# Kernel tuning notes

Hardware: AMD Instinct MI355X
Metric: run time of the kernel (lower is better)

Reference implementation:

```python
import jax, jax.numpy as jnp
import numpy as np

# Model dims
B, N, D_MODEL, N_HEADS = 8, 4096, 512, 8
EXPAND = 2
D1 = (EXPAND * D_MODEL) // N_HEADS * N_HEADS      # 1024
HEAD_DIM = D1 // N_HEADS                          # 128
RANK, NK = 32, 16
GAMMA = 0.999


def setup_inputs() -> dict:
    key = jax.random.key(0)
    ks = jax.random.split(key, 24)

    def p(i, shape, std=0.02):
        return std * jax.random.normal(ks[i], shape, dtype=jnp.float32)

    def toep_params(i0):
        # SKI low-rank Toeplitz operator params: kernel values at NK inducing
        # lag positions, factorized as (h, nk, r) @ (h, r, d), plus lag-0 term.
        return (p(i0, (N_HEADS, 1, HEAD_DIM), 1.0),        # zero lag
                p(i0 + 1, (N_HEADS, NK, RANK), 0.1),       # pos lags A
                p(i0 + 2, (N_HEADS, RANK, HEAD_DIM), 0.1), # pos lags B
                p(i0 + 3, (N_HEADS, NK, RANK), 0.1),       # neg lags A
                p(i0 + 4, (N_HEADS, RANK, HEAD_DIM), 0.1)) # neg lags B

    t1 = toep_params(7)
    t2 = toep_params(12)
    return {
        'x': jax.random.normal(ks[0], (B, N, D_MODEL), dtype=jnp.float32),
        'u_w': p(1, (D1, D_MODEL)), 'u_b': p(2, (D1,)),
        'v_w': p(3, (D1, D_MODEL)), 'v_b': p(4, (D1,)),
        'o_w': p(5, (D_MODEL, D1)), 'o_b': p(6, (D_MODEL,)),
        't1_zero': t1[0], 't1_pa': t1[1], 't1_pb': t1[2], 't1_na': t1[3], 't1_nb': t1[4],
        't2_zero': t2[0], 't2_pa': t2[1], 't2_pb': t2[2], 't2_na': t2[3], 't2_nb': t2[4],
    }


def _build_kernel(zero, pos_a, pos_b, neg_a, neg_b, n):
    """Build circular-conv kernel a of shape (h, 2n, d): a[k]=t(k), a[2n-k]=t(-k)."""
    h, nk, _ = pos_a.shape
    d = pos_b.shape[-1]
    tm_pos = jnp.einsum('hkr,hrd->hkd', pos_a, pos_b)   # kernel at inducing lags
    tm_neg = jnp.einsum('hkr,hrd->hkd', neg_a, neg_b)
    lags = jnp.arange(1, n, dtype=jnp.float32)          # lags 1..n-1
    # linear interpolation from NK inducing points to n-1 lags
    pos_f = (lags - 1.0) / max(n - 2, 1) * (nk - 1)
    lo = jnp.floor(pos_f).astype(jnp.int32)
    hi = jnp.minimum(lo + 1, nk - 1)
    w = (pos_f - lo)[None, :, None]
    decay = (GAMMA ** lags)[None, :, None]              # exponential decay bias
    t_pos = ((1.0 - w) * tm_pos[:, lo] + w * tm_pos[:, hi]) * decay
    t_neg = ((1.0 - w) * tm_neg[:, lo] + w * tm_neg[:, hi]) * decay
    return jnp.concatenate(
        [zero, t_pos, jnp.zeros((h, 1, d), t_pos.dtype), jnp.flip(t_neg, axis=1)],
        axis=1)


def _toep_apply(x, zero, pos_a, pos_b, neg_a, neg_b):
    # x: (b, n, g) with g = h*d; multi-head Toeplitz mixing along axis 1 via FFT.
    b, n, g = x.shape
    h = zero.shape[0]
    d = g // h
    xh = x.reshape(b, n, h, d).transpose(0, 2, 1, 3)    # (b, h, n, d)
    a = _build_kernel(zero, pos_a, pos_b, neg_a, neg_b, n)  # (h, 2n, d)
    y = jnp.fft.irfft(
        jnp.fft.rfft(xh, 2 * n, axis=2) * jnp.fft.rfft(a, axis=1)[None],
        2 * n, axis=2)[:, :, :n]
    return y.transpose(0, 2, 1, 3).reshape(b, n, g)


def reference(x, u_w, u_b, v_w, v_b, o_w, o_b,
              t1_zero, t1_pa, t1_pb, t1_na, t1_nb,
              t2_zero, t2_pa, t2_pb, t2_na, t2_nb):
    b, n, _ = x.shape
    H = int(np.sqrt(n))
    W = n // H
    u = jax.nn.silu(x @ u_w.T + u_b)
    v = jax.nn.silu(x @ v_w.T + v_b)
    g = v.shape[-1]
    t1 = (t1_zero, t1_pa, t1_pb, t1_na, t1_nb)
    t2 = (t2_zero, t2_pa, t2_pb, t2_na, t2_nb)
    # path 1: mix along W (rows) with toep1, then along H (cols) with toep2
    o1 = _toep_apply(v.reshape(b * H, W, g), *t1)
    o1 = o1.reshape(b, H, W, g).transpose(0, 2, 1, 3).reshape(b * W, H, g)
    o1 = _toep_apply(o1, *t2)
    o1 = o1.reshape(b, W, H, g).transpose(0, 2, 1, 3).reshape(b, H * W, g)
    # path 2: mix along H with toep2, then along W with toep1
    v2 = v.reshape(b, H, W, g).transpose(0, 2, 1, 3).reshape(b * W, H, g)
    o2 = _toep_apply(v2, *t2)
    o2 = o2.reshape(b, W, H, g).transpose(0, 2, 1, 3).reshape(b * H, W, g)
    o2 = _toep_apply(o2, *t1)
    o2 = o2.reshape(b, H * W, g)
    # SiLU gate + output projection
    return (u * (o1 + o2)) @ o_w.T + o_b
```

## Files before the change

### kernel.cpp

```cpp
#include <hip/hip_runtime.h>
#include <hip/hip_bf16.h>
#include <hip/hip_fp16.h>

typedef __bf16 bf16;
typedef bf16 bf16x2 __attribute__((ext_vector_type(2)));
typedef bf16 bf16x4 __attribute__((ext_vector_type(4)));
typedef bf16 bf16x8 __attribute__((ext_vector_type(8)));
typedef float f32x2 __attribute__((ext_vector_type(2)));
typedef float f32x4 __attribute__((ext_vector_type(4)));

__device__ __forceinline__ void gload_lds16(const void* g, void* l) {
  __builtin_amdgcn_global_load_lds((__attribute__((address_space(1))) void*)g,
                                   (__attribute__((address_space(3))) void*)l,
                                   16, 0, 0);
}

__device__ __forceinline__ f32x2 fma2(f32x2 a, f32x2 b, f32x2 c) {
  return __builtin_elementwise_fma(a, b, c);
}

__device__ __forceinline__ f32x2 cvt2(unsigned int u) {
  __half2 h = *(__half2*)&u;
  float2 f = __half22float2(h);
  f32x2 r = {f.x, f.y};
  return r;
}


__global__ void cast_f32_to_bf16(const float* __restrict__ in, bf16* __restrict__ out, int n4) {
  int i = blockIdx.x * blockDim.x + threadIdx.x;
  if (i >= n4) return;
  float4 v = ((const float4*)in)[i];
  bf16x4 o = {(bf16)v.x, (bf16)v.y, (bf16)v.z, (bf16)v.w};
  ((bf16x4*)out)[i] = o;
}

__global__ void cast_w3(const float* __restrict__ uw, const float* __restrict__ vw,
                        const float* __restrict__ ow,
                        bf16* __restrict__ wuv, bf16* __restrict__ owb) {
  int t = blockIdx.x * 256 + threadIdx.x;
  int r = t >> 17;
  int i = t & 131071;
  const float* src = (r == 0) ? uw : (r == 1) ? vw : ow;
  bf16* dst = (r == 2) ? owb : (wuv + (r == 1) * 524288);
  float4 v = ((const float4*)src)[i];
  bf16x4 o = {(bf16)v.x, (bf16)v.y, (bf16)v.z, (bf16)v.w};
  ((bf16x4*)dst)[i] = o;
}

__global__ void concat_bias(const float* __restrict__ ub, const float* __restrict__ vb,
                            float* __restrict__ buv) {
  int i = blockIdx.x * blockDim.x + threadIdx.x;
  if (i < 1024) { buv[i] = ub[i]; buv[1024 + i] = vb[i]; }
}

__global__ void build_tkp(const float* __restrict__ zero, const float* __restrict__ pa,
                          const float* __restrict__ pb, const float* __restrict__ na,
                          const float* __restrict__ nb, unsigned int* __restrict__ Tkp,
                          float scale) {
  int idx = blockIdx.x * blockDim.x + threadIdx.x;
  if (idx >= 8 * 127 * 64) return;
  int cp = idx & 63;
  int lagIdx = (idx >> 6) % 127;
  int h = idx / (64 * 127);
  int lag = lagIdx - 63;
  float t0, t1;
  if (lag == 0) {
    t0 = zero[h * 128 + 2 * cp];
    t1 = zero[h * 128 + 2 * cp + 1];
  } else {
    int k = lag > 0 ? lag : -lag;
    const float* A  = lag > 0 ? pa : na;
    const float* Bm = lag > 0 ? pb : nb;
    float pos_f = (float)(k - 1) * (15.0f / 62.0f);
    int lo = (int)floorf(pos_f);
    int hi = min(lo + 1, 15);
    float w = pos_f - (float)lo;
    float s0 = 0.f, s1 = 0.f;
    for (int r = 0; r < 32; ++r) {
      float c = (1.f - w) * A[(h * 16 + lo) * 32 + r] + w * A[(h * 16 + hi) * 32 + r];
      s0 += c * Bm[(h * 32 + r) * 128 + 2 * cp];
      s1 += c * Bm[(h * 32 + r) * 128 + 2 * cp + 1];
    }
    float dec = powf(0.999f, (float)k);
    t0 = s0 * dec;
    t1 = s1 * dec;
  }
  __half2 hv = __floats2half2_rn(t0 * scale, t1 * scale);
  Tkp[idx] = *(unsigned int*)&hv;
}


template<int MODE>
__global__ __launch_bounds__(256)
void gemm_bt(const bf16* __restrict__ A, const bf16* __restrict__ B,
             const float* __restrict__ bias,
             bf16* __restrict__ out_u, bf16* __restrict__ out_v,
             float* __restrict__ out_f,
             int M, int N, int K) {
  __shared__ bf16 As[128 * 32];
  __shared__ bf16 Bs[128 * 32];
  const int tid  = threadIdx.x;
  const int lane = tid & 63;
  const int nbn  = N >> 7;
  const int cpx  = gridDim.x >> 3;
  const int swz  = (blockIdx.x & 7) * cpx + (blockIdx.x >> 3);
  const int br   = (swz / nbn) << 7;
  const int bc   = (swz % nbn) << 7;
  const int wub  = __builtin_amdgcn_readfirstlane(tid & 192);

  f32x4 acc[4][4] = {};

  auto stage = [&](int k0) {
#pragma unroll
    for (int r = 0; r < 2; ++r) {
      const int flat = r * 256 + tid;
      const int row  = flat >> 2;
      const int kc   = (flat & 3) << 3;
      gload_lds16(A + ((size_t)(br + row) * K + k0 + kc),
                  (char*)As + (size_t)(r * 256 + wub) * 16);
      gload_lds16(B + ((size_t)(bc + row) * K + k0 + kc),
                  (char*)Bs + (size_t)(r * 256 + wub) * 16);
    }
  };

  const int l15 = lane & 15;
  const int lk  = (lane >> 4) << 3;
  const int wr  = ((tid >> 7) & 1) << 6;
  const int wc  = ((tid >> 6) & 1) << 6;

  auto compute = [&]() {
    bf16x8 af[4], bfr[4];
#pragma unroll
    for (int m = 0; m < 4; ++m)
      af[m] = *(const bf16x8*)&As[(wr + m * 16 + l15) * 32 + lk];
#pragma unroll
    for (int n = 0; n < 4; ++n)
      bfr[n] = *(const bf16x8*)&Bs[(wc + n * 16 + l15) * 32 + lk];
#pragma unroll
    for (int m = 0; m < 4; ++m)
#pragma unroll
      for (int n = 0; n < 4; ++n)
        acc[m][n] = __builtin_amdgcn_mfma_f32_16x16x32_bf16(af[m], bfr[n], acc[m][n], 0, 0, 0);
  };

  stage(0);
  __syncthreads();
  for (int k0 = 32; k0 < K; k0 += 32) {
    compute();
    __syncthreads();
    stage(k0);
    __syncthreads();
  }
  compute();

  const int lr4 = (lane >> 4) << 2;
  if (MODE == 0) {
    const bool isU = (bc < 1024);
    bf16* outp = isU ? out_u : out_v;
#pragma unroll
    for (int m = 0; m < 4; ++m) {
#pragma unroll
      for (int n = 0; n < 4; ++n) {
        const int col  = bc + wc + n * 16 + l15;
        const int ocol = (bc & 1023) + wc + n * 16 + l15;
        const float bv = bias[col];
#pragma unroll
        for (int r = 0; r < 4; ++r) {
          const int row = br + wr + m * 16 + lr4 + r;
          float xv = acc[m][n][r] + bv;
          float s  = xv / (1.f + __expf(-xv));
          outp[(size_t)row * 1024 + ocol] = (bf16)s;
        }
      }
    }
  } else {
#pragma unroll
    for (int m = 0; m < 4; ++m) {
#pragma unroll
      for (int n = 0; n < 4; ++n) {
        const int col  = bc + wc + n * 16 + l15;
        const float bv = bias[col];
#pragma unroll
        for (int r = 0; r < 4; ++r) {
          const int row = br + wr + m * 16 + lr4 + r;
          out_f[(size_t)row * N + col] = acc[m][n][r] + bv;
        }
      }
    }
  }
}


template<int FUSE>
__global__ __launch_bounds__(256)
void toep_pass(const bf16* __restrict__ in, const unsigned int* __restrict__ Tkp,
               const bf16* __restrict__ ufuse, bf16* __restrict__ out,
               int stride_j, int stride_row) {
  __shared__ unsigned int tkl[8192];
  __shared__ bf16 vbuf[64 * 132];
  const int tid    = threadIdx.x;
  const int rowIdx = blockIdx.x >> 3;
  const int head   = blockIdx.x & 7;
  const size_t base = (size_t)(rowIdx >> 6) * 4194304
                    + (size_t)(rowIdx & 63) * stride_row + head * 128;

  {
    const unsigned int* tg = Tkp + head * 8128;
    const int wub = __builtin_amdgcn_readfirstlane(tid & 192);
#pragma unroll
    for (int it = 0; it < 8; ++it) {
      const int flat = it * 256 + tid;
      gload_lds16(tg + flat * 4, (char*)tkl + (size_t)(it * 256 + wub) * 16);
    }
  }
#pragma unroll
  for (int it = 0; it < 2; ++it) {
    int c  = it * 256 + tid;
    int j  = c >> 3;
    int cg = c & 7;
    const bf16* p = in + base + (size_t)j * stride_j + cg * 16;
    bf16x8 a0 = *(const bf16x8*)p;
    bf16x8 a1 = *(const bf16x8*)(p + 8);
    *(bf16x8*)&vbuf[j * 132 + cg * 16]     = a0;
    *(bf16x8*)&vbuf[j * 132 + cg * 16 + 8] = a1;
  }
  __syncthreads();

  const int lane = tid & 63;
  const int i0   = (tid >> 6) << 4;
  f32x2 acc[16] = {};

  for (int jb = 0; jb < 4; ++jb) {
    f32x2 t[31];
    const int tbase = (i0 - 16 * jb + 48) * 64 + lane;
#pragma unroll
    for (int s = 0; s < 31; ++s) t[s] = cvt2(tkl[tbase + s * 64]);
#pragma unroll
    for (int jj = 0; jj < 16; ++jj) {
      unsigned int vu = *(const unsigned int*)&vbuf[(jb * 16 + jj) * 132 + (lane << 1)];
      f32x2 v2;
      v2.x = __uint_as_float(vu << 16);
      v2.y = __uint_as_float(vu & 0xFFFF0000u);
#pragma unroll
      for (int ii = 0; ii < 16; ++ii)
        acc[ii] = fma2(t[ii - jj + 15], v2, acc[ii]);
    }
  }

  const int d0 = lane << 1;
#pragma unroll
  for (int ii = 0; ii < 16; ++ii) {
    const size_t oidx = base + (size_t)(i0 + ii) * stride_j + d0;
    float a0 = acc[ii].x, a1 = acc[ii].y;
    if (FUSE) {
      bf16x2 uu = *(const bf16x2*)(ufuse + oidx);
      a0 *= (float)uu[0];
      a1 *= (float)uu[1];
    }
    bf16x2 o2 = {(bf16)a0, (bf16)a1};
    *(bf16x2*)(out + oidx) = o2;
  }
}


extern "C" void kernel_launch(void* const* d_in, const int* in_sizes, int n_in,
                              void* d_out, int out_size, void* d_ws, size_t ws_size,
                              hipStream_t stream) {
  const float* x    = (const float*)d_in[0];
  const float* u_w  = (const float*)d_in[1];
  const float* u_b  = (const float*)d_in[2];
  const float* v_w  = (const float*)d_in[3];
  const float* v_b  = (const float*)d_in[4];
  const float* o_w  = (const float*)d_in[5];
  const float* o_b  = (const float*)d_in[6];
  const float* t1z  = (const float*)d_in[7];
  const float* t1pa = (const float*)d_in[8];
  const float* t1pb = (const float*)d_in[9];
  const float* t1na = (const float*)d_in[10];
  const float* t1nb = (const float*)d_in[11];
  const float* t2z  = (const float*)d_in[12];
  const float* t2pa = (const float*)d_in[13];
  const float* t2pb = (const float*)d_in[14];
  const float* t2na = (const float*)d_in[15];
  const float* t2nb = (const float*)d_in[16];

  char* ws = (char*)d_ws;
  size_t off = 0;
  auto alloc = [&](size_t bytes) {
    char* p = ws + off;
    off += (bytes + 255) & ~(size_t)255;
    return p;
  };
  bf16*  xb   = (bf16*)alloc(32768ull * 512 * 2);
  bf16*  wuv  = (bf16*)alloc(2048ull * 512 * 2);
  bf16*  owb  = (bf16*)alloc(512ull * 1024 * 2);
  float* buv  = (float*)alloc(2048ull * 4);
  unsigned int* Tkp1 = (unsigned int*)alloc(8ull * 127 * 64 * 4 + 256);
  unsigned int* Tkp2 = (unsigned int*)alloc(8ull * 127 * 64 * 4 + 256);
  bf16*  u    = (bf16*)alloc(32768ull * 1024 * 2);
  bf16*  v    = (bf16*)alloc(32768ull * 1024 * 2);
  bf16*  tmid = (bf16*)alloc(32768ull * 1024 * 2);
  bf16*  g    = v;

  cast_f32_to_bf16<<<16384, 256, 0, stream>>>(x, xb, 16777216 / 4);
  cast_w3<<<1536, 256, 0, stream>>>(u_w, v_w, o_w, wuv, owb);
  concat_bias<<<4, 256, 0, stream>>>(u_b, v_b, buv);
  build_tkp<<<254, 256, 0, stream>>>(t1z, t1pa, t1pb, t1na, t1nb, Tkp1, 1.0f);
  build_tkp<<<254, 256, 0, stream>>>(t2z, t2pa, t2pb, t2na, t2nb, Tkp2, 2.0f);

  gemm_bt<0><<<4096, 256, 0, stream>>>(xb, wuv, buv, u, v, nullptr, 32768, 2048, 512);
  toep_pass<0><<<4096, 256, 0, stream>>>(v, Tkp1, nullptr, tmid, 1024, 65536);
  toep_pass<1><<<4096, 256, 0, stream>>>(tmid, Tkp2, u, g, 65536, 1024);
  gemm_bt<1><<<1024, 256, 0, stream>>>(g, owb, o_b, nullptr, nullptr, (float*)d_out,
                                       32768, 512, 1024);
}
```

Baseline: 309.0 us.

## Fuse first Toeplitz pass into the U/V projection GEMM epilogue

The V half of the input projection GEMM now keeps the SiLU-activated 128x128 tile in LDS and applies the first Toeplitz mixing pass directly, writing tmid instead of a full v buffer. This removes one kernel launch and a full write and read of the 32768x1024 v tensor. Each block's 128 rows hold two 64-row image rows, so the row-wise Toeplitz mixing can run within a single tile. The change also adds launch_bounds occupancy hints to both kernels, at the cost of a heavier GEMM epilogue with high register pressure and tail work only in the V blocks.

```diff
diff --git a/kernel.cpp b/kernel.cpp
--- a/kernel.cpp
+++ b/kernel.cpp
@@ -91,13 +91,143 @@
 }
 
 
-template<int MODE>
+#define VP 132
+
+__global__ __launch_bounds__(256, 3)
+void gemm_uvt(const bf16* __restrict__ A, const bf16* __restrict__ B,
+              const float* __restrict__ bias, const unsigned int* __restrict__ Tkp1,
+              bf16* __restrict__ out_u, bf16* __restrict__ tmid) {
+  __shared__ __align__(16) char smem[2 * 64 * VP * 2];
+  bf16* As = (bf16*)smem;
+  bf16* Bs = (bf16*)(smem + 8192);
+  bf16* vls = (bf16*)smem;
+  const int K = 512;
+  const int tid  = threadIdx.x;
+  const int lane = tid & 63;
+  const int cpx  = gridDim.x >> 3;
+  const int swz  = (blockIdx.x & 7) * cpx + (blockIdx.x >> 3);
+  const int br   = (swz >> 4) << 7;
+  const int bc   = (swz & 15) << 7;
+  const int wub  = __builtin_amdgcn_readfirstlane(tid & 192);
+
+  f32x4 acc[4][4] = {};
+
+  auto stage = [&](int k0) {
+#pragma unroll
+    for (int r = 0; r < 2; ++r) {
+      const int flat = r * 256 + tid;
+      const int row  = flat >> 2;
+      const int kc   = (flat & 3) << 3;
+      gload_lds16(A + ((size_t)(br + row) * K + k0 + kc),
+                  (char*)As + (size_t)(r * 256 + wub) * 16);
+      gload_lds16(B + ((size_t)(bc + row) * K + k0 + kc),
+                  (char*)Bs + (size_t)(r * 256 + wub) * 16);
+    }
+  };
+
+  const int l15 = lane & 15;
+  const int lk  = (lane >> 4) << 3;
+  const int wr  = ((tid >> 7) & 1) << 6;
+  const int wc  = ((tid >> 6) & 1) << 6;
+
+  auto compute = [&]() {
+    bf16x8 af[4], bfr[4];
+#pragma unroll
+    for (int m = 0; m < 4; ++m)
+      af[m] = *(const bf16x8*)&As[(wr + m * 16 + l15) * 32 + lk];
+#pragma unroll
+    for (int n = 0; n < 4; ++n)
+      bfr[n] = *(const bf16x8*)&Bs[(wc + n * 16 + l15) * 32 + lk];
+#pragma unroll
+    for (int m = 0; m < 4; ++m)
+#pragma unroll
+      for (int n = 0; n < 4; ++n)
+        acc[m][n] = __builtin_amdgcn_mfma_f32_16x16x32_bf16(af[m], bfr[n], acc[m][n], 0, 0, 0);
+  };
+
+  stage(0);
+  __syncthreads();
+  for (int k0 = 32; k0 < K; k0 += 32) {
+    compute();
+    __syncthreads();
+    stage(k0);
+    __syncthreads();
+  }
+  compute();
+  __syncthreads();
+
+  const int lr4 = (lane >> 4) << 2;
+  if (bc < 1024) {
+#pragma unroll
+    for (int m = 0; m < 4; ++m) {
+#pragma unroll
+      for (int n = 0; n < 4; ++n) {
+        const int col = bc + wc + n * 16 + l15;
+        const float bv = bias[col];
+#pragma unroll
+        for (int r = 0; r < 4; ++r) {
+          const int row = br + wr + m * 16 + lr4 + r;
+          float xv = acc[m][n][r] + bv;
+          float s  = xv / (1.f + __expf(-xv));
+          out_u[(size_t)row * 1024 + col] = (bf16)s;
+        }
+      }
+    }
+  } else {
+    const int head = (bc - 1024) >> 7;
+#pragma unroll
+    for (int m = 0; m < 4; ++m) {
+#pragma unroll
+      for (int n = 0; n < 4; ++n) {
+        const int col = wc + n * 16 + l15;
+        const float bv = bias[bc + col];
+#pragma unroll
+        for (int r = 0; r < 4; ++r) {
+          const int rin = wr + m * 16 + lr4 + r;
+          float xv = acc[m][n][r] + bv;
+          float s  = xv / (1.f + __expf(-xv));
+          vls[rin * VP + col] = (bf16)s;
+        }
+      }
+    }
+    __syncthreads();
+
+    const unsigned int* tg = Tkp1 + head * 8128;
+    const int i0 = (tid >> 6) << 4;
+    for (int ir = 0; ir < 2; ++ir) {
+      f32x2 acc2[16] = {};
+      for (int jb = 0; jb < 4; ++jb) {
+        f32x2 t[31];
+        const int tb = (i0 - 16 * jb + 48) * 64 + lane;
+#pragma unroll
+        for (int s = 0; s < 31; ++s) t[s] = cvt2(tg[tb + s * 64]);
+#pragma unroll
+        for (int jj = 0; jj < 16; ++jj) {
+          unsigned int vu =
+            *(const unsigned int*)&vls[(ir * 64 + jb * 16 + jj) * VP + (lane << 1)];
+          f32x2 v2;
+          v2.x = __uint_as_float(vu << 16);
+          v2.y = __uint_as_float(vu & 0xFFFF0000u);
+#pragma unroll
+          for (int ii = 0; ii < 16; ++ii)
+            acc2[ii] = fma2(t[ii - jj + 15], v2, acc2[ii]);
+        }
+      }
+      const size_t obase = (size_t)(br + ir * 64) * 1024 + (bc - 1024) + (lane << 1);
+#pragma unroll
+      for (int ii = 0; ii < 16; ++ii) {
+        bf16x2 o2 = {(bf16)acc2[ii].x, (bf16)acc2[ii].y};
+        *(bf16x2*)(tmid + obase + (size_t)(i0 + ii) * 1024) = o2;
+      }
+    }
+  }
+}
+
+
 __global__ __launch_bounds__(256)
-void gemm_bt(const bf16* __restrict__ A, const bf16* __restrict__ B,
-             const float* __restrict__ bias,
-             bf16* __restrict__ out_u, bf16* __restrict__ out_v,
-             float* __restrict__ out_f,
-             int M, int N, int K) {
+void gemm_bt1(const bf16* __restrict__ A, const bf16* __restrict__ B,
+              const float* __restrict__ bias, float* __restrict__ out_f,
+              int M, int N, int K) {
   __shared__ bf16 As[128 * 32];
   __shared__ bf16 Bs[128 * 32];
   const int tid  = threadIdx.x;
@@ -155,45 +285,24 @@
   compute();
 
   const int lr4 = (lane >> 4) << 2;
-  if (MODE == 0) {
-    const bool isU = (bc < 1024);
-    bf16* outp = isU ? out_u : out_v;
-#pragma unroll
-    for (int m = 0; m < 4; ++m) {
-#pragma unroll
-      for (int n = 0; n < 4; ++n) {
-        const int col  = bc + wc + n * 16 + l15;
-        const int ocol = (bc & 1023) + wc + n * 16 + l15;
-        const float bv = bias[col];
-#pragma unroll
-        for (int r = 0; r < 4; ++r) {
-          const int row = br + wr + m * 16 + lr4 + r;
-          float xv = acc[m][n][r] + bv;
-          float s  = xv / (1.f + __expf(-xv));
-          outp[(size_t)row * 1024 + ocol] = (bf16)s;
-        }
+#pragma unroll
+  for (int m = 0; m < 4; ++m) {
+#pragma unroll
+    for (int n = 0; n < 4; ++n) {
+      const int col = bc + wc + n * 16 + l15;
+      const float bv = bias[col];
+#pragma unroll
+      for (int r = 0; r < 4; ++r) {
+        const int row = br + wr + m * 16 + lr4 + r;
+        out_f[(size_t)row * N + col] = acc[m][n][r] + bv;
       }
     }
-  } else {
-#pragma unroll
-    for (int m = 0; m < 4; ++m) {
-#pragma unroll
-      for (int n = 0; n < 4; ++n) {
-        const int col  = bc + wc + n * 16 + l15;
-        const float bv = bias[col];
-#pragma unroll
-        for (int r = 0; r < 4; ++r) {
-          const int row = br + wr + m * 16 + lr4 + r;
-          out_f[(size_t)row * N + col] = acc[m][n][r] + bv;
-        }
-      }
-    }
   }
 }
 
 
 template<int FUSE>
-__global__ __launch_bounds__(256)
+__global__ __launch_bounds__(256, 2)
 void toep_pass(const bf16* __restrict__ in, const unsigned int* __restrict__ Tkp,
                const bf16* __restrict__ ufuse, bf16* __restrict__ out,
                int stride_j, int stride_row) {
@@ -299,9 +408,8 @@
   unsigned int* Tkp1 = (unsigned int*)alloc(8ull * 127 * 64 * 4 + 256);
   unsigned int* Tkp2 = (unsigned int*)alloc(8ull * 127 * 64 * 4 + 256);
   bf16*  u    = (bf16*)alloc(32768ull * 1024 * 2);
-  bf16*  v    = (bf16*)alloc(32768ull * 1024 * 2);
   bf16*  tmid = (bf16*)alloc(32768ull * 1024 * 2);
-  bf16*  g    = v;
+  bf16*  g    = (bf16*)alloc(32768ull * 1024 * 2);
 
   cast_f32_to_bf16<<<16384, 256, 0, stream>>>(x, xb, 16777216 / 4);
   cast_w3<<<1536, 256, 0, stream>>>(u_w, v_w, o_w, wuv, owb);
@@ -309,9 +417,7 @@
   build_tkp<<<254, 256, 0, stream>>>(t1z, t1pa, t1pb, t1na, t1nb, Tkp1, 1.0f);
   build_tkp<<<254, 256, 0, stream>>>(t2z, t2pa, t2pb, t2na, t2nb, Tkp2, 2.0f);
 
-  gemm_bt<0><<<4096, 256, 0, stream>>>(xb, wuv, buv, u, v, nullptr, 32768, 2048, 512);
-  toep_pass<0><<<4096, 256, 0, stream>>>(v, Tkp1, nullptr, tmid, 1024, 65536);
+  gemm_uvt<<<4096, 256, 0, stream>>>(xb, wuv, buv, Tkp1, u, tmid);
   toep_pass<1><<<4096, 256, 0, stream>>>(tmid, Tkp2, u, g, 65536, 1024);
-  gemm_bt<1><<<1024, 256, 0, stream>>>(g, owb, o_b, nullptr, nullptr, (float*)d_out,
-                                       32768, 512, 1024);
-}
+  gemm_bt1<<<1024, 256, 0, stream>>>(g, owb, o_b, (float*)d_out, 32768, 512, 1024);
+}
```

Result: slower. 417.9 us (+35.2%).

## Read fp32 Toeplitz kernel from global/L2 and stage fp32 inputs in LDS

Applied to the files above, without the earlier changes.

Toeplitz coefficients are now built and stored as fp32 instead of packed fp16, and toep_pass reads them straight from global memory (L2-cached) instead of copying a 32KB table into LDS per block. The input tile is converted to fp32 while being staged in LDS, which removes per-iteration bf16 unpacking and fp16 conversion. Launch bounds now request 4 blocks per SM, and LDS use drops, allowing more occupancy. In exchange, the inner loop depends on global load latency for the kernel values, and the fp32 vbuf doubles the LDS footprint of the input tile.

```diff
diff --git a/kernel.cpp b/kernel.cpp
--- a/kernel.cpp
+++ b/kernel.cpp
@@ -17,13 +17,6 @@
 
 __device__ __forceinline__ f32x2 fma2(f32x2 a, f32x2 b, f32x2 c) {
   return __builtin_elementwise_fma(a, b, c);
-}
-
-__device__ __forceinline__ f32x2 cvt2(unsigned int u) {
-  __half2 h = *(__half2*)&u;
-  float2 f = __half22float2(h);
-  f32x2 r = {f.x, f.y};
-  return r;
 }
 
 
@@ -54,20 +47,19 @@
   if (i < 1024) { buv[i] = ub[i]; buv[1024 + i] = vb[i]; }
 }
 
-__global__ void build_tkp(const float* __restrict__ zero, const float* __restrict__ pa,
+__global__ void build_tkf(const float* __restrict__ zero, const float* __restrict__ pa,
                           const float* __restrict__ pb, const float* __restrict__ na,
-                          const float* __restrict__ nb, unsigned int* __restrict__ Tkp,
+                          const float* __restrict__ nb, float* __restrict__ Tkf,
                           float scale) {
   int idx = blockIdx.x * blockDim.x + threadIdx.x;
-  if (idx >= 8 * 127 * 64) return;
-  int cp = idx & 63;
-  int lagIdx = (idx >> 6) % 127;
-  int h = idx / (64 * 127);
+  if (idx >= 8 * 127 * 128) return;
+  int d = idx & 127;
+  int lagIdx = (idx >> 7) % 127;
+  int h = idx / (128 * 127);
   int lag = lagIdx - 63;
-  float t0, t1;
+  float val;
   if (lag == 0) {
-    t0 = zero[h * 128 + 2 * cp];
-    t1 = zero[h * 128 + 2 * cp + 1];
+    val = zero[h * 128 + d];
   } else {
     int k = lag > 0 ? lag : -lag;
     const float* A  = lag > 0 ? pa : na;
@@ -76,18 +68,14 @@
     int lo = (int)floorf(pos_f);
     int hi = min(lo + 1, 15);
     float w = pos_f - (float)lo;
-    float s0 = 0.f, s1 = 0.f;
+    float s = 0.f;
     for (int r = 0; r < 32; ++r) {
       float c = (1.f - w) * A[(h * 16 + lo) * 32 + r] + w * A[(h * 16 + hi) * 32 + r];
-      s0 += c * Bm[(h * 32 + r) * 128 + 2 * cp];
-      s1 += c * Bm[(h * 32 + r) * 128 + 2 * cp + 1];
-    }
-    float dec = powf(0.999f, (float)k);
-    t0 = s0 * dec;
-    t1 = s1 * dec;
-  }
-  __half2 hv = __floats2half2_rn(t0 * scale, t1 * scale);
-  Tkp[idx] = *(unsigned int*)&hv;
+      s += c * Bm[(h * 32 + r) * 128 + d];
+    }
+    val = s * powf(0.999f, (float)k);
+  }
+  Tkf[idx] = val * scale;
 }
 
 
@@ -192,28 +180,20 @@
 }
 
 
+#define VROW 130
+
 template<int FUSE>
-__global__ __launch_bounds__(256)
-void toep_pass(const bf16* __restrict__ in, const unsigned int* __restrict__ Tkp,
+__global__ __launch_bounds__(256, 4)
+void toep_pass(const bf16* __restrict__ in, const float* __restrict__ Tkf,
                const bf16* __restrict__ ufuse, bf16* __restrict__ out,
                int stride_j, int stride_row) {
-  __shared__ unsigned int tkl[8192];
-  __shared__ bf16 vbuf[64 * 132];
+  __shared__ float vbuf[64 * VROW];
   const int tid    = threadIdx.x;
   const int rowIdx = blockIdx.x >> 3;
   const int head   = blockIdx.x & 7;
   const size_t base = (size_t)(rowIdx >> 6) * 4194304
                     + (size_t)(rowIdx & 63) * stride_row + head * 128;
 
-  {
-    const unsigned int* tg = Tkp + head * 8128;
-    const int wub = __builtin_amdgcn_readfirstlane(tid & 192);
-#pragma unroll
-    for (int it = 0; it < 8; ++it) {
-      const int flat = it * 256 + tid;
-      gload_lds16(tg + flat * 4, (char*)tkl + (size_t)(it * 256 + wub) * 16);
-    }
-  }
 #pragma unroll
   for (int it = 0; it < 2; ++it) {
     int c  = it * 256 + tid;
@@ -222,26 +202,31 @@
     const bf16* p = in + base + (size_t)j * stride_j + cg * 16;
     bf16x8 a0 = *(const bf16x8*)p;
     bf16x8 a1 = *(const bf16x8*)(p + 8);
-    *(bf16x8*)&vbuf[j * 132 + cg * 16]     = a0;
-    *(bf16x8*)&vbuf[j * 132 + cg * 16 + 8] = a1;
+    f32x4 f0 = {(float)a0[0], (float)a0[1], (float)a0[2], (float)a0[3]};
+    f32x4 f1 = {(float)a0[4], (float)a0[5], (float)a0[6], (float)a0[7]};
+    f32x4 f2 = {(float)a1[0], (float)a1[1], (float)a1[2], (float)a1[3]};
+    f32x4 f3 = {(float)a1[4], (float)a1[5], (float)a1[6], (float)a1[7]};
+    float* dst = &vbuf[j * VROW + cg * 16];
+    *(f32x4*)(dst)      = f0;
+    *(f32x4*)(dst + 4)  = f1;
+    *(f32x4*)(dst + 8)  = f2;
+    *(f32x4*)(dst + 12) = f3;
   }
   __syncthreads();
 
   const int lane = tid & 63;
   const int i0   = (tid >> 6) << 4;
+  const float* tg = Tkf + head * 127 * 128 + (lane << 1);
   f32x2 acc[16] = {};
 
   for (int jb = 0; jb < 4; ++jb) {
     f32x2 t[31];
-    const int tbase = (i0 - 16 * jb + 48) * 64 + lane;
-#pragma unroll
-    for (int s = 0; s < 31; ++s) t[s] = cvt2(tkl[tbase + s * 64]);
+    const float* tb = tg + (i0 - 16 * jb + 48) * 128;
+#pragma unroll
+    for (int s = 0; s < 31; ++s) t[s] = *(const f32x2*)(tb + s * 128);
 #pragma unroll
     for (int jj = 0; jj < 16; ++jj) {
-      unsigned int vu = *(const unsigned int*)&vbuf[(jb * 16 + jj) * 132 + (lane << 1)];
-      f32x2 v2;
-      v2.x = __uint_as_float(vu << 16);
-      v2.y = __uint_as_float(vu & 0xFFFF0000u);
+      f32x2 v2 = *(const f32x2*)&vbuf[(jb * 16 + jj) * VROW + (lane << 1)];
 #pragma unroll
       for (int ii = 0; ii < 16; ++ii)
         acc[ii] = fma2(t[ii - jj + 15], v2, acc[ii]);
@@ -296,8 +281,8 @@
   bf16*  wuv  = (bf16*)alloc(2048ull * 512 * 2);
   bf16*  owb  = (bf16*)alloc(512ull * 1024 * 2);
   float* buv  = (float*)alloc(2048ull * 4);
-  unsigned int* Tkp1 = (unsigned int*)alloc(8ull * 127 * 64 * 4 + 256);
-  unsigned int* Tkp2 = (unsigned int*)alloc(8ull * 127 * 64 * 4 + 256);
+  float* Tkf1 = (float*)alloc(8ull * 127 * 128 * 4);
+  float* Tkf2 = (float*)alloc(8ull * 127 * 128 * 4);
   bf16*  u    = (bf16*)alloc(32768ull * 1024 * 2);
   bf16*  v    = (bf16*)alloc(32768ull * 1024 * 2);
   bf16*  tmid = (bf16*)alloc(32768ull * 1024 * 2);
@@ -306,12 +291,12 @@
   cast_f32_to_bf16<<<16384, 256, 0, stream>>>(x, xb, 16777216 / 4);
   cast_w3<<<1536, 256, 0, stream>>>(u_w, v_w, o_w, wuv, owb);
   concat_bias<<<4, 256, 0, stream>>>(u_b, v_b, buv);
-  build_tkp<<<254, 256, 0, stream>>>(t1z, t1pa, t1pb, t1na, t1nb, Tkp1, 1.0f);
-  build_tkp<<<254, 256, 0, stream>>>(t2z, t2pa, t2pb, t2na, t2nb, Tkp2, 2.0f);
+  build_tkf<<<508, 256, 0, stream>>>(t1z, t1pa, t1pb, t1na, t1nb, Tkf1, 1.0f);
+  build_tkf<<<508, 256, 0, stream>>>(t2z, t2pa, t2pb, t2na, t2nb, Tkf2, 2.0f);
 
   gemm_bt<0><<<4096, 256, 0, stream>>>(xb, wuv, buv, u, v, nullptr, 32768, 2048, 512);
-  toep_pass<0><<<4096, 256, 0, stream>>>(v, Tkp1, nullptr, tmid, 1024, 65536);
-  toep_pass<1><<<4096, 256, 0, stream>>>(tmid, Tkp2, u, g, 65536, 1024);
+  toep_pass<0><<<4096, 256, 0, stream>>>(v, Tkf1, nullptr, tmid, 1024, 65536);
+  toep_pass<1><<<4096, 256, 0, stream>>>(tmid, Tkf2, u, g, 65536, 1024);
   gemm_bt<1><<<1024, 256, 0, stream>>>(g, owb, o_b, nullptr, nullptr, (float*)d_out,
                                        32768, 512, 1024);
 }
```

After: 347.0 us. 12.3% more time.
